# Performance work log

Measured on AMD Instinct MI355X. Metric: run time of the kernel, lower is better.

The kernel has to match this reference:

```python
import jax, jax.numpy as jnp
import numpy as np

B, N = 4, 1024            # batches, atoms per structure
IN_CH, OUT_CH = 16, 16
N_BASIS = 16
MAX_RADIUS = 3.5
BOX_L = 19.7              # cubic lattice constant -> ~24 neighbors/atom
GAMMA = MAX_RADIUS / N_BASIS
N_NORM = 24.0             # avg neighbor count, out /= sqrt(n_norm)


def _build_periodic_edges(seed=0):
    rng = np.random.default_rng(seed)
    pos = rng.uniform(0.0, BOX_L, (B, N, 3)).astype(np.float32)
    shifts = BOX_L * np.array([[i, j, k] for i in (-1, 0, 1)
                               for j in (-1, 0, 1) for k in (-1, 0, 1)],
                              dtype=np.float32)
    src_l, dst_l, vec_l = [], [], []
    r2 = MAX_RADIUS * MAX_RADIUS
    for z in range(B):
        p = pos[z]
        for s in shifts:  # 27 periodic images, chunked to keep memory small
            diff = (p[None, :, :] + s[None, None, :]) - p[:, None, :]  # [a,b,3] = image_b - a
            d2 = (diff * diff).sum(-1)
            a_idx, b_idx = np.nonzero(d2 < r2)
            dst_l.append((z * N + a_idx).astype(np.int32))
            src_l.append((z * N + b_idx).astype(np.int32))
            vec_l.append(diff[a_idx, b_idx])
    edge_src = np.concatenate(src_l)
    edge_dst = np.concatenate(dst_l)
    edge_vec = np.concatenate(vec_l).astype(np.float32)
    # original zeroes self-image displacements with |r| < 1e-10
    self_mask = np.linalg.norm(edge_vec, axis=-1) < 1e-10
    edge_vec[self_mask] = 0.0
    return edge_src, edge_dst, edge_vec


def setup_inputs() -> dict:
    key = jax.random.key(0)
    k1, k2 = jax.random.split(key)
    edge_src, edge_dst, edge_vec = _build_periodic_edges()
    x = jax.random.normal(k1, (B * N, IN_CH), dtype=jnp.float32)
    W = jax.random.normal(k2, (N_BASIS + 3, OUT_CH, IN_CH), dtype=jnp.float32) * 0.1
    return {
        "x": x,
        "W": W,
        "edge_vec": jnp.asarray(edge_vec),
        "edge_src": jnp.asarray(edge_src),
        "edge_dst": jnp.asarray(edge_dst),
    }


def reference(x, W, edge_vec, edge_src, edge_dst):
    # per-edge kernel features: gaussian radial basis + unit direction
    r = jnp.linalg.norm(edge_vec, axis=-1, keepdims=True)            # [E,1]
    centers = jnp.linspace(0.0, MAX_RADIUS, N_BASIS, dtype=x.dtype)
    basis = jnp.exp(-((r - centers) / GAMMA) ** 2)                   # [E,nb]
    rhat = jnp.where(r > 1e-10, edge_vec / jnp.maximum(r, 1e-10), 0.0)
    feat = jnp.concatenate([basis, rhat], axis=-1)                   # [E,nb+3]
    # per-edge kernel eval (kernels = self.kernel(radius) in the original)
    K = jnp.einsum('ef,foi->eoi', feat, W)                           # [E,out,in]
    # per-edge matvec + scatter-add over destination atoms
    msg = jnp.einsum('eoi,ei->eo', K, x[edge_src])                   # [E,out]
    out = jax.ops.segment_sum(msg, edge_dst, num_segments=x.shape[0])
    out = out / jnp.sqrt(jnp.asarray(N_NORM, x.dtype))               # n_norm ** 0.5
    return out.reshape(B, N, OUT_CH)
```

## Files before the change

### kernel.cpp

```cpp
#include <hip/hip_runtime.h>
#include <hip/hip_fp16.h>
#include <math.h>

#define IN_CH 16
#define OUT_CH 16
#define N_BASIS 16
#define N_FEAT 19
#define Y_STRIDE (N_FEAT * OUT_CH)
#define GAMMA_INV (16.0f / 3.5f)
#define CENTER_STEP (3.5f / 15.0f)
#define INV_SQRT_NNORM 0.20412414523193154f

__global__ __launch_bounds__(320) void precompute_y(
    const float* __restrict__ x, const float* __restrict__ W,
    __half* __restrict__ y, float* __restrict__ out) {
  __shared__ float xs[IN_CH];
  const int a = blockIdx.x;
  const int t = threadIdx.x;
  if (t < IN_CH) {
    xs[t] = x[a * IN_CH + t];
    out[a * OUT_CH + t] = 0.0f;
  }
  __syncthreads();
  if (t < Y_STRIDE) {
    const float4* w4 = (const float4*)(W + t * IN_CH);
    float acc = 0.f;
#pragma unroll
    for (int q = 0; q < 4; ++q) {
      float4 w = w4[q];
      acc += w.x * xs[4 * q + 0] + w.y * xs[4 * q + 1] +
             w.z * xs[4 * q + 2] + w.w * xs[4 * q + 3];
    }
    y[(size_t)a * Y_STRIDE + t] = __float2half(acc * INV_SQRT_NNORM);
  }
}

__global__ __launch_bounds__(256) void edge_scatter(
    const __half* __restrict__ y, const float* __restrict__ edge_vec,
    const int* __restrict__ edge_src, const int* __restrict__ edge_dst,
    float* __restrict__ out, int E) {
  __shared__ float feat[16][N_FEAT];
  __shared__ float msg[16][OUT_CH];
  __shared__ int dsts[16];

  const int t = threadIdx.x;
  const int eg = t >> 4;
  const int o = t & 15;
  const int e = blockIdx.x * 16 + eg;
  const bool valid = (e < E);

  float vx = 0.f, vy = 0.f, vz = 0.f;
  int src = 0;
  if (valid) {
    vx = edge_vec[3 * e + 0];
    vy = edge_vec[3 * e + 1];
    vz = edge_vec[3 * e + 2];
    src = edge_src[e];
    if (o == 0) dsts[eg] = edge_dst[e];
  } else if (o == 0) {
    dsts[eg] = -1 - eg;
  }
  const float r = sqrtf(vx * vx + vy * vy + vz * vz);

  const float tt = (r - CENTER_STEP * (float)o) * GAMMA_INV;
  feat[eg][o] = __expf(-tt * tt);
  if (o < 3) {
    const float inv = (r > 1e-10f) ? (1.0f / r) : 0.0f;
    const float comp = (o == 0) ? vx : ((o == 1) ? vy : vz);
    feat[eg][N_BASIS + o] = comp * inv;
  }
  __syncthreads();

  float acc = 0.f;
  if (valid) {
    const __half* __restrict__ yrow = y + (size_t)src * Y_STRIDE + o;
#pragma unroll
    for (int f = 0; f < N_FEAT; ++f)
      acc += feat[eg][f] * __half2float(yrow[f * OUT_CH]);
  }
  msg[eg][o] = acc;
  __syncthreads();

  const int mydst = dsts[eg];
  int leader = eg;
#pragma unroll
  for (int j = 0; j < 16; ++j) {
    if (dsts[j] == mydst) { leader = j; break; }
  }
  if (leader == eg && mydst >= 0) {
    float total = 0.f;
#pragma unroll
    for (int j = 0; j < 16; ++j) {
      if (j >= eg && dsts[j] == mydst) total += msg[j][o];
    }
    atomicAdd(&out[mydst * OUT_CH + o], total);
  }
}

__global__ __launch_bounds__(256) void edge_direct(
    const float* __restrict__ x, const float* __restrict__ W,
    const float* __restrict__ edge_vec, const int* __restrict__ edge_src,
    const int* __restrict__ edge_dst, float* __restrict__ out, int E) {
  __shared__ float Ws[N_FEAT * OUT_CH * IN_CH];
  __shared__ float feat[16][N_FEAT];
  __shared__ float xs[16][IN_CH];

  const int t = threadIdx.x;
  for (int i = t; i < N_FEAT * OUT_CH * IN_CH; i += 256) Ws[i] = W[i];

  const int eg = t >> 4;
  const int o = t & 15;
  const int e = blockIdx.x * 16 + eg;
  const bool valid = (e < E);

  float vx = 0.f, vy = 0.f, vz = 0.f;
  int src = 0, dst = 0;
  if (valid) {
    vx = edge_vec[3 * e + 0];
    vy = edge_vec[3 * e + 1];
    vz = edge_vec[3 * e + 2];
    src = edge_src[e];
    dst = edge_dst[e];
    xs[eg][o] = x[src * IN_CH + o];
  }
  const float r = sqrtf(vx * vx + vy * vy + vz * vz);
  const float tt = (r - CENTER_STEP * (float)o) * GAMMA_INV;
  feat[eg][o] = __expf(-tt * tt);
  if (o < 3) {
    const float inv = (r > 1e-10f) ? (1.0f / r) : 0.0f;
    const float comp = (o == 0) ? vx : ((o == 1) ? vy : vz);
    feat[eg][N_BASIS + o] = comp * inv;
  }
  __syncthreads();

  if (valid) {
    float acc = 0.f;
#pragma unroll
    for (int f = 0; f < N_FEAT; ++f) {
      const float* wrow = &Ws[(f * OUT_CH + o) * IN_CH];
      float dot = 0.f;
#pragma unroll
      for (int i = 0; i < IN_CH; ++i) dot += wrow[i] * xs[eg][i];
      acc += feat[eg][f] * dot;
    }
    atomicAdd(&out[dst * OUT_CH + o], acc * INV_SQRT_NNORM);
  }
}

extern "C" void kernel_launch(void* const* d_in, const int* in_sizes, int n_in,
                              void* d_out, int out_size, void* d_ws,
                              size_t ws_size, hipStream_t stream) {
  const float* x = (const float*)d_in[0];
  const float* W = (const float*)d_in[1];
  const float* edge_vec = (const float*)d_in[2];
  const int* edge_src = (const int*)d_in[3];
  const int* edge_dst = (const int*)d_in[4];
  float* out = (float*)d_out;

  const int E = in_sizes[3];
  const int n_atoms = in_sizes[0] / IN_CH;

  const size_t y_bytes = (size_t)n_atoms * Y_STRIDE * sizeof(__half);
  if (ws_size >= y_bytes) {
    __half* y = (__half*)d_ws;
    precompute_y<<<n_atoms, 320, 0, stream>>>(x, W, y, out);
    edge_scatter<<<(E + 15) / 16, 256, 0, stream>>>(y, edge_vec, edge_src,
                                                    edge_dst, out, E);
  } else {
    hipMemsetAsync(out, 0, (size_t)out_size * sizeof(float), stream);
    edge_direct<<<(E + 15) / 16, 256, 0, stream>>>(x, W, edge_vec, edge_src,
                                                   edge_dst, out, E);
  }
}
```

Before: 81.28 us.

## Batch atoms per block in precompute and process two channels per thread in scatter

precompute_y now handles 16 atoms per block and keeps each thread's W row in registers, so the weights are reused across atoms and 16x fewer blocks are launched. edge_scatter handles 32 edges per block with each thread computing two output channels through half2 loads. This halves the threads per edge and doubles work per thread. Duplicate-destination merging is now done only within 16-edge groups. The aim is to cut launch and block overhead and per-edge load instructions, at the cost of more work per thread.

```diff
diff --git a/kernel.cpp b/kernel.cpp
--- a/kernel.cpp
+++ b/kernel.cpp
@@ -10,28 +10,41 @@
 #define GAMMA_INV (16.0f / 3.5f)
 #define CENTER_STEP (3.5f / 15.0f)
 #define INV_SQRT_NNORM 0.20412414523193154f
+#define APB 16
+#define EPB 32
 
 __global__ __launch_bounds__(320) void precompute_y(
     const float* __restrict__ x, const float* __restrict__ W,
-    __half* __restrict__ y, float* __restrict__ out) {
-  __shared__ float xs[IN_CH];
-  const int a = blockIdx.x;
+    __half* __restrict__ y, float* __restrict__ out, int n_atoms) {
+  __shared__ float xs[APB][IN_CH];
   const int t = threadIdx.x;
-  if (t < IN_CH) {
-    xs[t] = x[a * IN_CH + t];
-    out[a * OUT_CH + t] = 0.0f;
-  }
-  __syncthreads();
+  const int a0 = blockIdx.x * APB;
+
+  if (t < APB * IN_CH) {
+    const int idx = a0 * IN_CH + t;
+    const bool ok = idx < n_atoms * IN_CH;
+    xs[t >> 4][t & 15] = ok ? x[idx] : 0.0f;
+    if (ok) out[idx] = 0.0f;
+  }
+
+  float4 w0, w1, w2, w3;
   if (t < Y_STRIDE) {
     const float4* w4 = (const float4*)(W + t * IN_CH);
-    float acc = 0.f;
-#pragma unroll
-    for (int q = 0; q < 4; ++q) {
-      float4 w = w4[q];
-      acc += w.x * xs[4 * q + 0] + w.y * xs[4 * q + 1] +
-             w.z * xs[4 * q + 2] + w.w * xs[4 * q + 3];
-    }
-    y[(size_t)a * Y_STRIDE + t] = __float2half(acc * INV_SQRT_NNORM);
+    w0 = w4[0]; w1 = w4[1]; w2 = w4[2]; w3 = w4[3];
+  }
+  __syncthreads();
+
+  if (t < Y_STRIDE) {
+#pragma unroll
+    for (int al = 0; al < APB; ++al) {
+      if (a0 + al >= n_atoms) break;
+      const float* xv = xs[al];
+      float acc = w0.x * xv[0] + w0.y * xv[1] + w0.z * xv[2] + w0.w * xv[3] +
+                  w1.x * xv[4] + w1.y * xv[5] + w1.z * xv[6] + w1.w * xv[7] +
+                  w2.x * xv[8] + w2.y * xv[9] + w2.z * xv[10] + w2.w * xv[11] +
+                  w3.x * xv[12] + w3.y * xv[13] + w3.z * xv[14] + w3.w * xv[15];
+      y[(size_t)(a0 + al) * Y_STRIDE + t] = __float2half(acc * INV_SQRT_NNORM);
+    }
   }
 }
 
@@ -39,14 +52,17 @@
     const __half* __restrict__ y, const float* __restrict__ edge_vec,
     const int* __restrict__ edge_src, const int* __restrict__ edge_dst,
     float* __restrict__ out, int E) {
-  __shared__ float feat[16][N_FEAT];
-  __shared__ float msg[16][OUT_CH];
-  __shared__ int dsts[16];
+  __shared__ float feat[EPB][20];
+  __shared__ float msg[EPB][OUT_CH];
+  __shared__ int dsts[EPB];
 
   const int t = threadIdx.x;
-  const int eg = t >> 4;
-  const int o = t & 15;
-  const int e = blockIdx.x * 16 + eg;
+  const int w = t >> 7;
+  const int rem = t & 127;
+  const int el = rem & 15;
+  const int h = rem >> 4;
+  const int s = w * 16 + el;
+  const int e = blockIdx.x * EPB + s;
   const bool valid = (e < E);
 
   float vx = 0.f, vy = 0.f, vz = 0.f;
@@ -56,44 +72,57 @@
     vy = edge_vec[3 * e + 1];
     vz = edge_vec[3 * e + 2];
     src = edge_src[e];
-    if (o == 0) dsts[eg] = edge_dst[e];
-  } else if (o == 0) {
-    dsts[eg] = -1 - eg;
+    if (h == 0) dsts[s] = edge_dst[e];
+  } else if (h == 0) {
+    dsts[s] = -1 - s;
   }
   const float r = sqrtf(vx * vx + vy * vy + vz * vz);
 
-  const float tt = (r - CENTER_STEP * (float)o) * GAMMA_INV;
-  feat[eg][o] = __expf(-tt * tt);
-  if (o < 3) {
+  const float t0 = (r - CENTER_STEP * (float)(2 * h)) * GAMMA_INV;
+  const float t1 = (r - CENTER_STEP * (float)(2 * h + 1)) * GAMMA_INV;
+  feat[s][2 * h] = __expf(-t0 * t0);
+  feat[s][2 * h + 1] = __expf(-t1 * t1);
+  if (h < 3) {
     const float inv = (r > 1e-10f) ? (1.0f / r) : 0.0f;
-    const float comp = (o == 0) ? vx : ((o == 1) ? vy : vz);
-    feat[eg][N_BASIS + o] = comp * inv;
-  }
-  __syncthreads();
-
-  float acc = 0.f;
-  if (valid) {
-    const __half* __restrict__ yrow = y + (size_t)src * Y_STRIDE + o;
-#pragma unroll
-    for (int f = 0; f < N_FEAT; ++f)
-      acc += feat[eg][f] * __half2float(yrow[f * OUT_CH]);
-  }
-  msg[eg][o] = acc;
-  __syncthreads();
-
-  const int mydst = dsts[eg];
-  int leader = eg;
-#pragma unroll
-  for (int j = 0; j < 16; ++j) {
-    if (dsts[j] == mydst) { leader = j; break; }
-  }
-  if (leader == eg && mydst >= 0) {
-    float total = 0.f;
-#pragma unroll
-    for (int j = 0; j < 16; ++j) {
-      if (j >= eg && dsts[j] == mydst) total += msg[j][o];
-    }
-    atomicAdd(&out[mydst * OUT_CH + o], total);
+    const float comp = (h == 0) ? vx : ((h == 1) ? vy : vz);
+    feat[s][N_BASIS + h] = comp * inv;
+  }
+  __syncthreads();
+
+  float a0 = 0.f, a1 = 0.f;
+  if (valid) {
+    const __half2* __restrict__ yrow =
+        (const __half2*)(y + (size_t)src * Y_STRIDE + 2 * h);
+#pragma unroll
+    for (int f = 0; f < N_FEAT; ++f) {
+      const float2 yv = __half22float2(yrow[f * (OUT_CH / 2)]);
+      const float ff = feat[s][f];
+      a0 += ff * yv.x;
+      a1 += ff * yv.y;
+    }
+  }
+  msg[s][2 * h] = a0;
+  msg[s][2 * h + 1] = a1;
+  __syncthreads();
+
+  const int wb = w * 16;
+  const int mydst = dsts[s];
+  int leader = el;
+#pragma unroll
+  for (int k = 0; k < 16; ++k) {
+    if (dsts[wb + k] == mydst) { leader = k; break; }
+  }
+  if (leader == el && mydst >= 0) {
+    float s0 = 0.f, s1 = 0.f;
+#pragma unroll
+    for (int k = 0; k < 16; ++k) {
+      if (k >= el && dsts[wb + k] == mydst) {
+        s0 += msg[wb + k][2 * h];
+        s1 += msg[wb + k][2 * h + 1];
+      }
+    }
+    atomicAdd(&out[mydst * OUT_CH + 2 * h], s0);
+    atomicAdd(&out[mydst * OUT_CH + 2 * h + 1], s1);
   }
 }
 
@@ -163,9 +192,10 @@
   const size_t y_bytes = (size_t)n_atoms * Y_STRIDE * sizeof(__half);
   if (ws_size >= y_bytes) {
     __half* y = (__half*)d_ws;
-    precompute_y<<<n_atoms, 320, 0, stream>>>(x, W, y, out);
-    edge_scatter<<<(E + 15) / 16, 256, 0, stream>>>(y, edge_vec, edge_src,
-                                                    edge_dst, out, E);
+    precompute_y<<<(n_atoms + APB - 1) / APB, 320, 0, stream>>>(x, W, y, out,
+                                                               n_atoms);
+    edge_scatter<<<(E + EPB - 1) / EPB, 256, 0, stream>>>(y, edge_vec, edge_src,
+                                                          edge_dst, out, E);
   } else {
     hipMemsetAsync(out, 0, (size_t)out_size * sizeof(float), stream);
     edge_direct<<<(E + 15) / 16, 256, 0, stream>>>(x, W, edge_vec, edge_src,
```

New measurement: 90.31 us. +11.1%, slower.
